# Optimization experiments

Measured on AMD Instinct MI355X. Metric: run time of the kernel, lower is better.

Reference implementation:

```python
import jax, jax.numpy as jnp
import numpy as np

B, DIM, MID, H, W = 4, 256, 128, 128, 128
EPS = 1e-5


def _conv(x, w, pad):
    # x: [B,C,H,W], w: [O,I,k,k]
    return jax.lax.conv_general_dilated(
        x, w, window_strides=(1, 1), padding=[(pad, pad), (pad, pad)],
        dimension_numbers=('NCHW', 'OIHW', 'NCHW'))


def _bn(x, g, b, m, v):
    inv = jax.lax.rsqrt(v + EPS)
    scale = (g * inv)[None, :, None, None]
    shift = (b - m * g * inv)[None, :, None, None]
    return x * scale + shift


def _convbnrelu(x, w, g, b, m, v):
    return jax.nn.relu(_bn(_conv(x, w, 1), g, b, m, v))


# CornerNet directional pools: sequential max-accumulation scans.
def top_pool(x):     # max over y' >= y  -> reversed cummax along H
    return jax.lax.cummax(x, axis=2, reverse=True)

def bottom_pool(x):  # max over y' <= y
    return jax.lax.cummax(x, axis=2)

def left_pool(x):    # max over x' >= x
    return jax.lax.cummax(x, axis=3, reverse=True)

def right_pool(x):   # max over x' <= x
    return jax.lax.cummax(x, axis=3)


def setup_inputs() -> dict:
    key = jax.random.key(0)
    ks = jax.random.split(key, 32)
    it = iter(ks)

    def w(shape, scale=0.05):
        return jax.random.normal(next(it), shape, jnp.float32) * scale

    def bn_params(c):
        return (jnp.ones((c,), jnp.float32) + 0.1 * jax.random.normal(next(it), (c,), jnp.float32),
                0.1 * jax.random.normal(next(it), (c,), jnp.float32),
                0.1 * jax.random.normal(next(it), (c,), jnp.float32),
                jax.random.uniform(next(it), (c,), jnp.float32) + 0.5)

    inp = {'x': jax.random.normal(next(it), (B, DIM, H, W), jnp.float32)}

    inp['p1_w'] = w((MID, DIM, 3, 3))
    inp['p1_g'], inp['p1_b'], inp['p1_m'], inp['p1_v'] = bn_params(MID)
    inp['p2_w'] = w((MID, DIM, 3, 3))
    inp['p2_g'], inp['p2_b'], inp['p2_m'], inp['p2_v'] = bn_params(MID)
    inp['p_w'] = w((DIM, MID, 3, 3))
    inp['p_g'], inp['p_b'], inp['p_m'], inp['p_v'] = bn_params(DIM)
    inp['c1_w'] = w((DIM, DIM, 1, 1))
    inp['c1_g'], inp['c1_b'], inp['c1_m'], inp['c1_v'] = bn_params(DIM)
    inp['c2_w'] = w((DIM, DIM, 3, 3))
    inp['c2_g'], inp['c2_b'], inp['c2_m'], inp['c2_v'] = bn_params(DIM)
    return inp


def reference(x,
              p1_w, p1_g, p1_b, p1_m, p1_v,
              p2_w, p2_g, p2_b, p2_m, p2_v,
              p_w, p_g, p_b, p_m, p_v,
              c1_w, c1_g, c1_b, c1_m, c1_v,
              c2_w, c2_g, c2_b, c2_m, c2_v):
    # branch 1: conv-bn-relu -> top pool -> bottom pool
    pool1 = bottom_pool(top_pool(_convbnrelu(x, p1_w, p1_g, p1_b, p1_m, p1_v)))
    # branch 2: conv-bn-relu -> left pool -> right pool
    pool2 = right_pool(left_pool(_convbnrelu(x, p2_w, p2_g, p2_b, p2_m, p2_v)))
    # merge branch
    p_bn1 = _bn(_conv(pool1 + pool2, p_w, 1), p_g, p_b, p_m, p_v)
    # skip branch: 1x1 conv + bn
    bn1 = _bn(_conv(x, c1_w, 0), c1_g, c1_b, c1_m, c1_v)
    # residual add + relu, then final conv-bn-relu
    return _convbnrelu(jax.nn.relu(p_bn1 + bn1), c2_w, c2_g, c2_b, c2_m, c2_v)
```

## Files before the change

### kernel.cpp

```cpp
#include <hip/hip_runtime.h>
#include <hip/hip_bf16.h>
#include <math.h>


constexpr int NB   = 4;
constexpr int CDIM = 256;
constexpr int CMID = 128;
constexpr int HS   = 128;
constexpr int WS   = 128;
constexpr float EPS = 1e-5f;

typedef __bf16 bf16x8 __attribute__((ext_vector_type(8)));
typedef float  f32x4  __attribute__((ext_vector_type(4)));

#define AS1 __attribute__((address_space(1)))
#define AS3 __attribute__((address_space(3)))

__device__ __forceinline__ void load16_lds(const void* gsrc, void* ldst) {
    __builtin_amdgcn_global_load_lds((const AS1 unsigned int*)gsrc,
                                     (AS3 unsigned int*)ldst, 16, 0, 0);
}

__global__ __launch_bounds__(512) void k_xprep(const float* __restrict__ xin,
                                               __hip_bfloat16* __restrict__ Xc)
{
    const int y = blockIdx.x;
    const int b = blockIdx.y;
    const int t = threadIdx.x;
    __shared__ __hip_bfloat16 lds[128 * 264];
#pragma unroll
    for (int k = 0; k < 16; ++k) {
        int idx = t + k * 512;
        int ci = idx >> 5, x4 = idx & 31;
        f32x4 v = *(const f32x4*)(xin + (((size_t)b * CDIM + ci) * HS + y) * WS + x4 * 4);
#pragma unroll
        for (int j = 0; j < 4; ++j)
            lds[(x4 * 4 + j) * 264 + ci] = __float2bfloat16(v[j]);
    }
    __syncthreads();
#pragma unroll
    for (int k = 0; k < 8; ++k) {
        int i = t + k * 512;
        int x = i >> 5, c8 = i & 31;
        bf16x8 vv = *(const bf16x8*)(lds + x * 264 + c8 * 8);
        *(bf16x8*)(Xc + ((size_t)(b * 128 + y) * 128 + x) * 256 + c8 * 8) = vv;
    }
}

__global__ __launch_bounds__(256) void k_wprep_all(
    const float* __restrict__ p1w, const float* __restrict__ p2w,
    const float* __restrict__ c2w, const float* __restrict__ c1w,
    __hip_bfloat16* __restrict__ Aw1, __hip_bfloat16* __restrict__ Aw2,
    __hip_bfloat16* __restrict__ Aw5, __hip_bfloat16* __restrict__ Aw4)
{
    const int bid = blockIdx.x;
    const int t   = threadIdx.x;
    if (bid < 512) {
        const float* W; __hip_bfloat16* A; int co;
        if (bid < 128)      { W = p1w; A = Aw1; co = bid; }
        else if (bid < 256) { W = p2w; A = Aw2; co = bid - 128; }
        else                { W = c2w; A = Aw5; co = bid - 256; }
#pragma unroll
        for (int tap = 0; tap < 9; ++tap)
            A[(size_t)co * 2304 + tap * 256 + t] =
                __float2bfloat16(W[((size_t)co * CDIM + t) * 9 + tap]);
    } else {
        int base = (bid - 512) * 512 + t;
        Aw4[base]       = __float2bfloat16(c1w[base]);
        Aw4[base + 256] = __float2bfloat16(c1w[base + 256]);
    }
}

template<int MODE>
__global__ __launch_bounds__(256, 2) void k_conv3(
    const __hip_bfloat16* __restrict__ Xc,
    const __hip_bfloat16* __restrict__ AwA, const __hip_bfloat16* __restrict__ AwB,
    const float* __restrict__ zbuf,
    const float* __restrict__ g1, const float* __restrict__ b1,
    const float* __restrict__ m1, const float* __restrict__ v1,
    const float* __restrict__ g2, const float* __restrict__ b2,
    const float* __restrict__ m2, const float* __restrict__ v2,
    float* __restrict__ out0, unsigned* __restrict__ cmax,
    unsigned* __restrict__ rmax, int CO)
{
    const int y0     = blockIdx.x * 2;
    const int branch = blockIdx.y;
    const int b      = blockIdx.z;
    const int co0    = (MODE == 0) ? branch * 128 : 0;

    const __hip_bfloat16* Aw = (MODE == 1 && branch) ? AwB : AwA;
    const float* gg  = (MODE == 1 && branch) ? g2 : g1;
    const float* bbp = (MODE == 1 && branch) ? b2 : b1;
    const float* mmp = (MODE == 1 && branch) ? m2 : m1;
    const float* vvp = (MODE == 1 && branch) ? v2 : v1;

    __shared__ __hip_bfloat16 smem[644 * 32];
    __shared__ float s_sc[128], s_sh[128];
    __shared__ unsigned s_red[2][128];
    char* smb = (char*)smem;

    const int t    = threadIdx.x;
    const int lane = t & 63;
    const int w    = t >> 6;
    const int ml   = lane & 15;
    const int q    = lane >> 4;
    const int mbase = (w >> 1) * 64;
    const int nbase = (w & 1) * 64;

    if (t < 128) {
        int co = co0 + t;
        float iv = rsqrtf(vvp[co] + EPS);
        float sc = gg[co] * iv;
        s_sc[t] = sc;
        s_sh[t] = bbp[co] - mmp[co] * sc;
        if (MODE == 1) { s_red[0][t] = 0u; s_red[1][t] = 0u; }
    }

    f32x4 acc[2][4][4];
#pragma unroll
    for (int yy = 0; yy < 2; ++yy)
#pragma unroll
        for (int mt = 0; mt < 4; ++mt)
#pragma unroll
            for (int nt = 0; nt < 4; ++nt)
                acc[yy][mt][nt] = (f32x4){0.f, 0.f, 0.f, 0.f};

    const __hip_bfloat16* bbase = Xc + (size_t)(b * 128) * 128 * 256;

#pragma unroll 1
    for (int ky = 0; ky < 3; ++ky) {
        const int yd0 = y0 + ky - 1;
        const __hip_bfloat16* arow = Aw + (size_t)co0 * 2304 + (3 * ky) * 256;
#pragma unroll 1
        for (int cih = 0; cih < 8; ++cih) {
            const int cb = cih * 32;
#pragma unroll
            for (int p = 0; p < 11; ++p) {
                int i = t + p * 256;
                if (i < 2576) {
                    int row = i >> 2, c = i & 3;
                    const __hip_bfloat16* src;
                    if (row < 384) {
                        int j = row >> 7, col = row & 127;
                        src = arow + (size_t)col * 2304 + j * 256 + cb + c * 8;
                    } else {
                        int rbi = row - 384;
                        int yy  = rbi >= 130;
                        int xi  = rbi - 130 * yy;
                        int gy  = yd0 + yy, gx = xi - 1;
                        src = ((unsigned)gy < 128u && (unsigned)gx < 128u)
                            ? bbase + ((size_t)(gy * 128 + gx)) * 256 + cb + c * 8
                            : (const __hip_bfloat16*)((const char*)zbuf + c * 16);
                    }
                    load16_lds(src, smb + (size_t)i * 16);
                }
            }
            __syncthreads();
#pragma unroll
            for (int j = 0; j < 3; ++j) {
                bf16x8 af[4];
#pragma unroll
                for (int mt = 0; mt < 4; ++mt)
                    af[mt] = *(const bf16x8*)(smb +
                        (size_t)(j * 128 + mbase + mt * 16 + ml) * 64 + q * 16);
#pragma unroll
                for (int yy = 0; yy < 2; ++yy) {
                    bf16x8 bfv[4];
#pragma unroll
                    for (int nt = 0; nt < 4; ++nt)
                        bfv[nt] = *(const bf16x8*)(smb +
                            (size_t)(384 + yy * 130 + nbase + nt * 16 + ml + j) * 64 + q * 16);
#pragma unroll
                    for (int mt = 0; mt < 4; ++mt)
#pragma unroll
                        for (int nt = 0; nt < 4; ++nt)
                            acc[yy][mt][nt] = __builtin_amdgcn_mfma_f32_16x16x32_bf16(
                                af[mt], bfv[nt], acc[yy][mt][nt], 0, 0, 0);
                }
            }
            __syncthreads();
        }
    }

#pragma unroll
    for (int mt = 0; mt < 4; ++mt) {
#pragma unroll
        for (int r = 0; r < 4; ++r) {
            const int col = mbase + mt * 16 + q * 4 + r;
            const float sc = s_sc[col], sh = s_sh[col];
            const int co = co0 + col;
            unsigned rmx0 = 0u, rmx1 = 0u;
#pragma unroll
            for (int nt = 0; nt < 4; ++nt) {
                float va = fmaxf(acc[0][mt][nt][r] * sc + sh, 0.f);
                float vb = fmaxf(acc[1][mt][nt][r] * sc + sh, 0.f);
                const int x = nbase + nt * 16 + ml;
                if (MODE == 0) {
                    out0[(((size_t)b * CO + co) * HS + y0)     * WS + x] = va;
                    out0[(((size_t)b * CO + co) * HS + y0 + 1) * WS + x] = vb;
                } else if (branch == 0) {
                    atomicMax(cmax + ((size_t)(b * 128 + co)) * 128 + x,
                              __float_as_uint(fmaxf(va, vb)));
                } else {
                    rmx0 = max(rmx0, __float_as_uint(va));
                    rmx1 = max(rmx1, __float_as_uint(vb));
                }
            }
            if (MODE == 1 && branch == 1) {
                atomicMax(&s_red[0][col], rmx0);
                atomicMax(&s_red[1][col], rmx1);
            }
        }
    }
    if (MODE == 1 && branch == 1) {
        __syncthreads();
        if (t < 128) {
            atomicMax(rmax + ((size_t)(b * 128 + t)) * 128 + y0,     s_red[0][t]);
            atomicMax(rmax + ((size_t)(b * 128 + t)) * 128 + y0 + 1, s_red[1][t]);
        }
    }
}

__global__ __launch_bounds__(128) void k_uv(
    const float* __restrict__ pw, const float* __restrict__ cm,
    const float* __restrict__ rm,
    __hip_bfloat16* __restrict__ U, __hip_bfloat16* __restrict__ V)
{
    const int co   = blockIdx.x;
    const int b    = blockIdx.y;
    const int mode = blockIdx.z;
    const int p    = threadIdx.x;
    float acc0 = 0.f, acc1 = 0.f, acc2 = 0.f;
    const float* base = (mode == 0) ? cm : rm;
    for (int ci = 0; ci < CMID; ++ci) {
        const float* w9 = pw + (co * CMID + ci) * 9;
        float s0[3], s1[3], s2[3];
        if (mode == 0) {
#pragma unroll
            for (int k = 0; k < 3; ++k) {
                float a = w9[k], qq = w9[3 + k], r = w9[6 + k];
                s0[k] = qq + r; s1[k] = a + qq + r; s2[k] = a + qq;
            }
        } else {
#pragma unroll
            for (int k = 0; k < 3; ++k) {
                float a = w9[k*3 + 0], qq = w9[k*3 + 1], r = w9[k*3 + 2];
                s0[k] = qq + r; s1[k] = a + qq + r; s2[k] = a + qq;
            }
        }
        const float* v = base + (b * CMID + ci) * 128;
#pragma unroll
        for (int k = 0; k < 3; ++k) {
            int pos = p + k - 1;
            if ((unsigned)pos < 128u) {
                float vv = v[pos];
                acc0 += s0[k] * vv; acc1 += s1[k] * vv; acc2 += s2[k] * vv;
            }
        }
    }
    __hip_bfloat16* dst = (mode == 0) ? U : V;
    dst[((0 * NB + b) * CDIM + co) * 128 + p] = __float2bfloat16(acc0);
    dst[((1 * NB + b) * CDIM + co) * 128 + p] = __float2bfloat16(acc1);
    dst[((2 * NB + b) * CDIM + co) * 128 + p] = __float2bfloat16(acc2);
}

__global__ __launch_bounds__(256, 3) void k_merge_mfma(
    const __hip_bfloat16* __restrict__ Xc, const __hip_bfloat16* __restrict__ Aw4,
    const __hip_bfloat16* __restrict__ U, const __hip_bfloat16* __restrict__ V,
    const float* __restrict__ pg, const float* __restrict__ pb,
    const float* __restrict__ pm, const float* __restrict__ pv,
    const float* __restrict__ cg, const float* __restrict__ cb,
    const float* __restrict__ cmn, const float* __restrict__ cv,
    __hip_bfloat16* __restrict__ Rc)
{
    const int y   = blockIdx.x;
    const int cot = blockIdx.y;
    const int b   = blockIdx.z;
    const int co0 = cot * 128;
    __shared__ __hip_bfloat16 smem[256 * 64];
    __shared__ float s_psc[128], s_psh[128], s_csc[128], s_csh[128];
    __shared__ float s_v0[128], s_vm[128], s_v1[128];
    char* smb = (char*)smem;
    const int t = threadIdx.x, lane = t & 63, w = t >> 6;
    const int ml = lane & 15, q = lane >> 4;
    const int mbase = (w >> 1) * 64, nbase = (w & 1) * 64;
    const int yc = (y == 0) ? 0 : ((y == HS - 1) ? 2 : 1);

    if (t < 128) {
        int co = co0 + t;
        float iv = rsqrtf(pv[co] + EPS);
        float psc = pg[co] * iv;
        s_psc[t] = psc;
        s_psh[t] = pb[co] - pm[co] * psc;
        float iv2 = rsqrtf(cv[co] + EPS);
        float csc = cg[co] * iv2;
        s_csc[t] = csc;
        s_csh[t] = cb[co] - cmn[co] * csc;
        const size_t vb = ((size_t)b * CDIM + co) * 128 + y;
        const size_t cstr = (size_t)NB * CDIM * 128;
        s_v0[t] = __bfloat162float(V[vb]);
        s_vm[t] = __bfloat162float(V[cstr + vb]);
        s_v1[t] = __bfloat162float(V[2 * cstr + vb]);
    }

    f32x4 acc[4][4];
#pragma unroll
    for (int mt = 0; mt < 4; ++mt)
#pragma unroll
        for (int nt = 0; nt < 4; ++nt)
            acc[mt][nt] = (f32x4){0.f, 0.f, 0.f, 0.f};

    const __hip_bfloat16* brow = Xc + (size_t)(b * 128 + y) * 128 * 256;
#pragma unroll 1
    for (int ks = 0; ks < 4; ++ks) {
        const __hip_bfloat16* ab = Aw4 + (size_t)co0 * 256 + ks * 64;
        const __hip_bfloat16* bb = brow + ks * 64;
#pragma unroll
        for (int p = 0; p < 8; ++p) {
            int i   = t + p * 256;
            int row = i >> 3;
            int c   = (i & 7) ^ (row & 7);
            const __hip_bfloat16* src = (row < 128)
                ? ab + (size_t)row * 256 + c * 8
                : bb + (size_t)(row - 128) * 256 + c * 8;
            load16_lds(src, smb + (size_t)i * 16);
        }
        __syncthreads();
#pragma unroll
        for (int s = 0; s < 2; ++s) {
            const int coff = ((s * 4 + q) ^ (ml & 7)) * 16;
            bf16x8 af[4], bfv[4];
#pragma unroll
            for (int mt = 0; mt < 4; ++mt)
                af[mt] = *(const bf16x8*)(smb + (size_t)(mbase + mt * 16 + ml) * 128 + coff);
#pragma unroll
            for (int nt = 0; nt < 4; ++nt)
                bfv[nt] = *(const bf16x8*)(smb + (size_t)(128 + nbase + nt * 16 + ml) * 128 + coff);
#pragma unroll
            for (int mt = 0; mt < 4; ++mt)
#pragma unroll
                for (int nt = 0; nt < 4; ++nt)
                    acc[mt][nt] = __builtin_amdgcn_mfma_f32_16x16x32_bf16(
                        af[mt], bfv[nt], acc[mt][nt], 0, 0, 0);
        }
        __syncthreads();
    }

    const __hip_bfloat16* Ub = U + ((size_t)(yc * NB + b) * CDIM + co0) * 128;
#pragma unroll
    for (int p = 0; p < 8; ++p) {
        int i = t + p * 256;
        load16_lds(Ub + (size_t)i * 8, smb + (size_t)i * 16);
    }
    __syncthreads();

#pragma unroll
    for (int mt = 0; mt < 4; ++mt) {
#pragma unroll
        for (int nt = 0; nt < 4; ++nt) {
            const int x = nbase + nt * 16 + ml;
            unsigned long long pk = 0;
#pragma unroll
            for (int r = 0; r < 4; ++r) {
                const int col = mbase + mt * 16 + q * 4 + r;
                float u  = __bfloat162float(smem[col * 128 + x]);
                float vt = (x == 0) ? s_v0[col] : ((x == WS - 1) ? s_v1[col] : s_vm[col]);
                float val = fmaxf((u + vt) * s_psc[col] + s_psh[col]
                                  + acc[mt][nt][r] * s_csc[col] + s_csh[col], 0.f);
                __hip_bfloat16 hb = __float2bfloat16(val);
                unsigned short bits;
                __builtin_memcpy(&bits, &hb, 2);
                pk |= (unsigned long long)bits << (16 * r);
            }
            *(unsigned long long*)((char*)Rc +
                ((size_t)((b * 128 + y) * 128 + x) * 256 + co0 + mbase + mt * 16 + q * 4) * 2) = pk;
        }
    }
}

extern "C" void kernel_launch(void* const* d_in, const int* in_sizes, int n_in,
                              void* d_out, int out_size, void* d_ws, size_t ws_size,
                              hipStream_t stream)
{
    (void)in_sizes; (void)n_in; (void)out_size; (void)ws_size;
    const float* x    = (const float*)d_in[0];
    const float* p1_w = (const float*)d_in[1];
    const float* p1_g = (const float*)d_in[2];
    const float* p1_b = (const float*)d_in[3];
    const float* p1_m = (const float*)d_in[4];
    const float* p1_v = (const float*)d_in[5];
    const float* p2_w = (const float*)d_in[6];
    const float* p2_g = (const float*)d_in[7];
    const float* p2_b = (const float*)d_in[8];
    const float* p2_m = (const float*)d_in[9];
    const float* p2_v = (const float*)d_in[10];
    const float* p_w  = (const float*)d_in[11];
    const float* p_g  = (const float*)d_in[12];
    const float* p_b  = (const float*)d_in[13];
    const float* p_m  = (const float*)d_in[14];
    const float* p_v  = (const float*)d_in[15];
    const float* c1_w = (const float*)d_in[16];
    const float* c1_g = (const float*)d_in[17];
    const float* c1_b = (const float*)d_in[18];
    const float* c1_m = (const float*)d_in[19];
    const float* c1_v = (const float*)d_in[20];
    const float* c2_w = (const float*)d_in[21];
    const float* c2_g = (const float*)d_in[22];
    const float* c2_b = (const float*)d_in[23];
    const float* c2_m = (const float*)d_in[24];
    const float* c2_v = (const float*)d_in[25];
    float* out = (float*)d_out;
    char* ws = (char*)d_ws;

    __hip_bfloat16* Xc   = (__hip_bfloat16*)ws;
    __hip_bfloat16* Rc   = (__hip_bfloat16*)(ws + 33554432);
    __hip_bfloat16* Ubuf = (__hip_bfloat16*)(ws + 67108864);
    __hip_bfloat16* Vbuf = (__hip_bfloat16*)(ws + 67895296);
    __hip_bfloat16* Aw1  = (__hip_bfloat16*)(ws + 67108864);
    __hip_bfloat16* Aw2  = (__hip_bfloat16*)(ws + 67698688);
    __hip_bfloat16* Aw5  = (__hip_bfloat16*)(ws + 68681728);
    __hip_bfloat16* Aw4  = (__hip_bfloat16*)(ws + 69861376);
    unsigned*       cmaxU = (unsigned*)(ws + 69992448);
    unsigned*       rmaxU = (unsigned*)(ws + 70254592);
    float*          zbuf  = (float*)(ws + 70516736);

    hipMemsetAsync(ws + 69992448, 0, 524544, stream);
    k_xprep<<<dim3(128, 4), 512, 0, stream>>>(x, Xc);
    k_wprep_all<<<dim3(640), 256, 0, stream>>>(
        p1_w, p2_w, c2_w, c1_w, Aw1, Aw2, Aw5, Aw4);

    k_conv3<1><<<dim3(64, 2, 4), 256, 0, stream>>>(
        Xc, Aw1, Aw2, zbuf,
        p1_g, p1_b, p1_m, p1_v, p2_g, p2_b, p2_m, p2_v,
        nullptr, cmaxU, rmaxU, CMID);

    k_uv<<<dim3(256, 4, 2), 128, 0, stream>>>(
        p_w, (const float*)cmaxU, (const float*)rmaxU, Ubuf, Vbuf);

    k_merge_mfma<<<dim3(128, 2, 4), 256, 0, stream>>>(
        Xc, Aw4, Ubuf, Vbuf, p_g, p_b, p_m, p_v,
        c1_g, c1_b, c1_m, c1_v, Rc);

    k_conv3<0><<<dim3(64, 2, 4), 256, 0, stream>>>(
        Rc, Aw5, nullptr, zbuf,
        c2_g, c2_b, c2_m, c2_v, nullptr, nullptr, nullptr, nullptr,
        out, nullptr, nullptr, CDIM);
}
```

Measured before the change: 392.7 us.

## Swizzle conv3 LDS layout, widen merge tile to all channels, fold memset into prep

Applies an XOR swizzle to the LDS chunk layout of the 3x3 conv kernel so fragment reads hit fewer bank conflicts. The merge kernel now has each block compute all 256 output channels for a row instead of splitting them across two blocks, so each X row is loaded once. This doubles the accumulators per thread and lowers the occupancy hint from 3 to 2. The hipMemsetAsync for the max buffers is replaced by extra zeroing blocks in the weight-prep kernel, which removes one launch.

```diff
diff --git a/kernel.cpp b/kernel.cpp
--- a/kernel.cpp
+++ b/kernel.cpp
@@ -51,7 +51,8 @@
     const float* __restrict__ p1w, const float* __restrict__ p2w,
     const float* __restrict__ c2w, const float* __restrict__ c1w,
     __hip_bfloat16* __restrict__ Aw1, __hip_bfloat16* __restrict__ Aw2,
-    __hip_bfloat16* __restrict__ Aw5, __hip_bfloat16* __restrict__ Aw4)
+    __hip_bfloat16* __restrict__ Aw5, __hip_bfloat16* __restrict__ Aw4,
+    f32x4* __restrict__ zdst)
 {
     const int bid = blockIdx.x;
     const int t   = threadIdx.x;
@@ -64,10 +65,14 @@
         for (int tap = 0; tap < 9; ++tap)
             A[(size_t)co * 2304 + tap * 256 + t] =
                 __float2bfloat16(W[((size_t)co * CDIM + t) * 9 + tap]);
-    } else {
+    } else if (bid < 640) {
         int base = (bid - 512) * 512 + t;
         Aw4[base]       = __float2bfloat16(c1w[base]);
         Aw4[base + 256] = __float2bfloat16(c1w[base + 256]);
+    } else if (bid < 768) {
+        zdst[(size_t)(bid - 640) * 256 + t] = (f32x4){0.f, 0.f, 0.f, 0.f};
+    } else {
+        if (t < 16) zdst[32768 + t] = (f32x4){0.f, 0.f, 0.f, 0.f};
     }
 }
 
@@ -138,7 +143,8 @@
             for (int p = 0; p < 11; ++p) {
                 int i = t + p * 256;
                 if (i < 2576) {
-                    int row = i >> 2, c = i & 3;
+                    int row = i >> 2, sl = i & 3;
+                    int c = sl ^ ((row >> 1) & 3);
                     const __hip_bfloat16* src;
                     if (row < 384) {
                         int j = row >> 7, col = row & 127;
@@ -160,16 +166,20 @@
             for (int j = 0; j < 3; ++j) {
                 bf16x8 af[4];
 #pragma unroll
-                for (int mt = 0; mt < 4; ++mt)
-                    af[mt] = *(const bf16x8*)(smb +
-                        (size_t)(j * 128 + mbase + mt * 16 + ml) * 64 + q * 16);
+                for (int mt = 0; mt < 4; ++mt) {
+                    const int ra = j * 128 + mbase + mt * 16 + ml;
+                    const int sa = q ^ ((ra >> 1) & 3);
+                    af[mt] = *(const bf16x8*)(smb + (size_t)ra * 64 + sa * 16);
+                }
 #pragma unroll
                 for (int yy = 0; yy < 2; ++yy) {
                     bf16x8 bfv[4];
 #pragma unroll
-                    for (int nt = 0; nt < 4; ++nt)
-                        bfv[nt] = *(const bf16x8*)(smb +
-                            (size_t)(384 + yy * 130 + nbase + nt * 16 + ml + j) * 64 + q * 16);
+                    for (int nt = 0; nt < 4; ++nt) {
+                        const int rb = 384 + yy * 130 + nbase + nt * 16 + ml + j;
+                        const int sb = q ^ ((rb >> 1) & 3);
+                        bfv[nt] = *(const bf16x8*)(smb + (size_t)rb * 64 + sb * 16);
+                    }
 #pragma unroll
                     for (int mt = 0; mt < 4; ++mt)
 #pragma unroll
@@ -264,7 +274,7 @@
     dst[((2 * NB + b) * CDIM + co) * 128 + p] = __float2bfloat16(acc2);
 }
 
-__global__ __launch_bounds__(256, 3) void k_merge_mfma(
+__global__ __launch_bounds__(256, 2) void k_merge_mfma(
     const __hip_bfloat16* __restrict__ Xc, const __hip_bfloat16* __restrict__ Aw4,
     const __hip_bfloat16* __restrict__ U, const __hip_bfloat16* __restrict__ V,
     const float* __restrict__ pg, const float* __restrict__ pb,
@@ -273,107 +283,110 @@
     const float* __restrict__ cmn, const float* __restrict__ cv,
     __hip_bfloat16* __restrict__ Rc)
 {
-    const int y   = blockIdx.x;
-    const int cot = blockIdx.y;
-    const int b   = blockIdx.z;
-    const int co0 = cot * 128;
-    __shared__ __hip_bfloat16 smem[256 * 64];
-    __shared__ float s_psc[128], s_psh[128], s_csc[128], s_csh[128];
-    __shared__ float s_v0[128], s_vm[128], s_v1[128];
+    const int y = blockIdx.x;
+    const int b = blockIdx.y;
+    __shared__ __hip_bfloat16 smem[32768];
+    __shared__ float s_psc[256], s_psh[256], s_csc[256], s_csh[256];
+    __shared__ float s_v0[256], s_vm[256], s_v1[256];
     char* smb = (char*)smem;
     const int t = threadIdx.x, lane = t & 63, w = t >> 6;
     const int ml = lane & 15, q = lane >> 4;
-    const int mbase = (w >> 1) * 64, nbase = (w & 1) * 64;
+    const int mbase = w * 64;
     const int yc = (y == 0) ? 0 : ((y == HS - 1) ? 2 : 1);
 
-    if (t < 128) {
-        int co = co0 + t;
+    {
+        int co = t;
         float iv = rsqrtf(pv[co] + EPS);
         float psc = pg[co] * iv;
-        s_psc[t] = psc;
-        s_psh[t] = pb[co] - pm[co] * psc;
+        s_psc[co] = psc;
+        s_psh[co] = pb[co] - pm[co] * psc;
         float iv2 = rsqrtf(cv[co] + EPS);
         float csc = cg[co] * iv2;
-        s_csc[t] = csc;
-        s_csh[t] = cb[co] - cmn[co] * csc;
+        s_csc[co] = csc;
+        s_csh[co] = cb[co] - cmn[co] * csc;
         const size_t vb = ((size_t)b * CDIM + co) * 128 + y;
         const size_t cstr = (size_t)NB * CDIM * 128;
-        s_v0[t] = __bfloat162float(V[vb]);
-        s_vm[t] = __bfloat162float(V[cstr + vb]);
-        s_v1[t] = __bfloat162float(V[2 * cstr + vb]);
-    }
-
-    f32x4 acc[4][4];
+        s_v0[co] = __bfloat162float(V[vb]);
+        s_vm[co] = __bfloat162float(V[cstr + vb]);
+        s_v1[co] = __bfloat162float(V[2 * cstr + vb]);
+    }
+
+    f32x4 acc[4][8];
 #pragma unroll
     for (int mt = 0; mt < 4; ++mt)
 #pragma unroll
-        for (int nt = 0; nt < 4; ++nt)
+        for (int nt = 0; nt < 8; ++nt)
             acc[mt][nt] = (f32x4){0.f, 0.f, 0.f, 0.f};
 
     const __hip_bfloat16* brow = Xc + (size_t)(b * 128 + y) * 128 * 256;
 #pragma unroll 1
     for (int ks = 0; ks < 4; ++ks) {
-        const __hip_bfloat16* ab = Aw4 + (size_t)co0 * 256 + ks * 64;
-        const __hip_bfloat16* bb = brow + ks * 64;
-#pragma unroll
-        for (int p = 0; p < 8; ++p) {
+#pragma unroll
+        for (int p = 0; p < 12; ++p) {
             int i   = t + p * 256;
-            int row = i >> 3;
-            int c   = (i & 7) ^ (row & 7);
-            const __hip_bfloat16* src = (row < 128)
-                ? ab + (size_t)row * 256 + c * 8
-                : bb + (size_t)(row - 128) * 256 + c * 8;
+            int row = i >> 3, sl = i & 7;
+            int c   = sl ^ (row & 7);
+            const __hip_bfloat16* src = (row < 256)
+                ? Aw4 + (size_t)row * 256 + ks * 64 + c * 8
+                : brow + (size_t)(row - 256) * 256 + ks * 64 + c * 8;
             load16_lds(src, smb + (size_t)i * 16);
         }
         __syncthreads();
 #pragma unroll
         for (int s = 0; s < 2; ++s) {
-            const int coff = ((s * 4 + q) ^ (ml & 7)) * 16;
-            bf16x8 af[4], bfv[4];
+            bf16x8 af[4], bfv[8];
+#pragma unroll
+            for (int mt = 0; mt < 4; ++mt) {
+                const int ra = mbase + mt * 16 + ml;
+                const int coff = ((s * 4 + q) ^ (ra & 7)) * 16;
+                af[mt] = *(const bf16x8*)(smb + (size_t)ra * 128 + coff);
+            }
+#pragma unroll
+            for (int nt = 0; nt < 8; ++nt) {
+                const int rb = 256 + nt * 16 + ml;
+                const int coff = ((s * 4 + q) ^ (rb & 7)) * 16;
+                bfv[nt] = *(const bf16x8*)(smb + (size_t)rb * 128 + coff);
+            }
 #pragma unroll
             for (int mt = 0; mt < 4; ++mt)
-                af[mt] = *(const bf16x8*)(smb + (size_t)(mbase + mt * 16 + ml) * 128 + coff);
-#pragma unroll
-            for (int nt = 0; nt < 4; ++nt)
-                bfv[nt] = *(const bf16x8*)(smb + (size_t)(128 + nbase + nt * 16 + ml) * 128 + coff);
-#pragma unroll
-            for (int mt = 0; mt < 4; ++mt)
-#pragma unroll
-                for (int nt = 0; nt < 4; ++nt)
+#pragma unroll
+                for (int nt = 0; nt < 8; ++nt)
                     acc[mt][nt] = __builtin_amdgcn_mfma_f32_16x16x32_bf16(
                         af[mt], bfv[nt], acc[mt][nt], 0, 0, 0);
         }
         __syncthreads();
     }
 
-    const __hip_bfloat16* Ub = U + ((size_t)(yc * NB + b) * CDIM + co0) * 128;
-#pragma unroll
-    for (int p = 0; p < 8; ++p) {
-        int i = t + p * 256;
-        load16_lds(Ub + (size_t)i * 8, smb + (size_t)i * 16);
+    const __hip_bfloat16* Ub = U + ((size_t)(yc * NB + b) * CDIM + mbase) * 128;
+#pragma unroll
+    for (int k = 0; k < 16; ++k) {
+        int i = lane + k * 64;
+        load16_lds(Ub + (size_t)i * 8, smb + (size_t)w * 16384 + (size_t)i * 16);
     }
     __syncthreads();
+    const __hip_bfloat16* ulds = smem + w * 8192;
 
 #pragma unroll
     for (int mt = 0; mt < 4; ++mt) {
 #pragma unroll
-        for (int nt = 0; nt < 4; ++nt) {
-            const int x = nbase + nt * 16 + ml;
+        for (int nt = 0; nt < 8; ++nt) {
+            const int x = nt * 16 + ml;
             unsigned long long pk = 0;
 #pragma unroll
             for (int r = 0; r < 4; ++r) {
-                const int col = mbase + mt * 16 + q * 4 + r;
-                float u  = __bfloat162float(smem[col * 128 + x]);
-                float vt = (x == 0) ? s_v0[col] : ((x == WS - 1) ? s_v1[col] : s_vm[col]);
-                float val = fmaxf((u + vt) * s_psc[col] + s_psh[col]
-                                  + acc[mt][nt][r] * s_csc[col] + s_csh[col], 0.f);
+                const int cl = mt * 16 + q * 4 + r;
+                const int co = mbase + cl;
+                float u  = __bfloat162float(ulds[cl * 128 + x]);
+                float vt = (x == 0) ? s_v0[co] : ((x == WS - 1) ? s_v1[co] : s_vm[co]);
+                float val = fmaxf((u + vt) * s_psc[co] + s_psh[co]
+                                  + acc[mt][nt][r] * s_csc[co] + s_csh[co], 0.f);
                 __hip_bfloat16 hb = __float2bfloat16(val);
                 unsigned short bits;
                 __builtin_memcpy(&bits, &hb, 2);
                 pk |= (unsigned long long)bits << (16 * r);
             }
             *(unsigned long long*)((char*)Rc +
-                ((size_t)((b * 128 + y) * 128 + x) * 256 + co0 + mbase + mt * 16 + q * 4) * 2) = pk;
+                ((size_t)((b * 128 + y) * 128 + x) * 256 + mbase + mt * 16 + q * 4) * 2) = pk;
         }
     }
 }
@@ -424,10 +437,9 @@
     unsigned*       rmaxU = (unsigned*)(ws + 70254592);
     float*          zbuf  = (float*)(ws + 70516736);
 
-    hipMemsetAsync(ws + 69992448, 0, 524544, stream);
+    k_wprep_all<<<dim3(769), 256, 0, stream>>>(
+        p1_w, p2_w, c2_w, c1_w, Aw1, Aw2, Aw5, Aw4, (f32x4*)(ws + 69992448));
     k_xprep<<<dim3(128, 4), 512, 0, stream>>>(x, Xc);
-    k_wprep_all<<<dim3(640), 256, 0, stream>>>(
-        p1_w, p2_w, c2_w, c1_w, Aw1, Aw2, Aw5, Aw4);
 
     k_conv3<1><<<dim3(64, 2, 4), 256, 0, stream>>>(
         Xc, Aw1, Aw2, zbuf,
@@ -437,7 +449,7 @@
     k_uv<<<dim3(256, 4, 2), 128, 0, stream>>>(
         p_w, (const float*)cmaxU, (const float*)rmaxU, Ubuf, Vbuf);
 
-    k_merge_mfma<<<dim3(128, 2, 4), 256, 0, stream>>>(
+    k_merge_mfma<<<dim3(128, 4), 256, 0, stream>>>(
         Xc, Aw4, Ubuf, Vbuf, p_g, p_b, p_m, p_v,
         c1_g, c1_b, c1_m, c1_v, Rc);
 
```

Result: no change. 390.6 us (-0.5%).
